# Kernel optimization log

Measured on AMD Instinct MI355X. Metric: run time of the kernel, lower is better.

Reference implementation:

```python
import jax, jax.numpy as jnp
import numpy as np
import math

HIDDEN = 4096
NUM_HEADS = 32
HEAD_DIM = HIDDEN // NUM_HEADS  # 128
SCALE = 1.0 / HEAD_DIM          # JAIS uses 1/d, not 1/sqrt(d)


def _alibi_slopes(n_heads: int) -> np.ndarray:
    cp2 = 2 ** math.floor(math.log2(n_heads))
    base = 2 ** (-2 ** (-(math.log2(cp2) - 3)))
    slopes = base ** np.arange(1, cp2 + 1, dtype=np.float32)
    if cp2 != n_heads:
        extra_base = 2 ** (-2 ** (-(math.log2(2 * cp2) - 3)))
        n_rem = min(cp2, n_heads - cp2)
        extra = extra_base ** np.arange(1, 1 + 2 * n_rem, 2, dtype=np.float32)
        slopes = np.concatenate([slopes, extra])
    return slopes.astype(np.float32)


def setup_inputs() -> dict:
    key = jax.random.key(0)
    k1, k2, k3, k4, k5 = jax.random.split(key, 5)
    B, S = 2, 2048
    return {
        "hidden_states": jax.random.normal(k1, (B, S, HIDDEN), dtype=jnp.float32),
        "w_attn": jax.random.normal(k2, (HIDDEN, 3 * HIDDEN), dtype=jnp.float32) * 0.02,
        "b_attn": jnp.zeros((3 * HIDDEN,), dtype=jnp.float32),
        "w_proj": jax.random.normal(k3, (HIDDEN, HIDDEN), dtype=jnp.float32) * 0.02,
        "b_proj": jnp.zeros((HIDDEN,), dtype=jnp.float32),
    }


def reference(hidden_states, w_attn, b_attn, w_proj, b_proj):
    B, S, _ = hidden_states.shape
    H, D = NUM_HEADS, HEAD_DIM

    # c_attn: fused QKV projection
    qkv = hidden_states @ w_attn + b_attn            # [B, S, 3*HIDDEN]
    q, k, v = jnp.split(qkv, 3, axis=-1)
    q = q.reshape(B, S, H, D)
    k = k.reshape(B, S, H, D)
    v = v.reshape(B, S, H, D)

    # attention scores with 1/d scaling
    scores = jnp.einsum("bqhd,bkhd->bhqk", q, k) * SCALE  # [B, H, S, S]

    # ALiBi bias: slope_h * (j - i), causal mask j <= i
    slopes = jnp.asarray(_alibi_slopes(H))                # [H]
    pos = jnp.arange(S)
    rel = pos[None, :] - pos[:, None]                     # j - i, [S, S]
    bias = slopes[:, None, None] * rel[None, :, :]        # [H, S, S]
    causal = rel <= 0
    scores = jnp.where(causal[None, None], scores + bias[None], -jnp.inf)

    attn = jax.nn.softmax(scores, axis=-1)
    out = jnp.einsum("bhqk,bkhd->bqhd", attn, v).reshape(B, S, HIDDEN)

    # c_proj
    return out @ w_proj + b_proj
```

## Files before the change

kernel.cpp:

```cpp
#include <hip/hip_runtime.h>
#include <hip/hip_bf16.h>
#include <cstdint>
#include <cstddef>

#define HIDDEN_ 4096
#define NHEAD 32
#define HDIM 128
#define SEQ 2048
#define BATCH 2
#define MROWS (BATCH * SEQ)
#define QKVN (3 * HIDDEN_)

typedef __bf16 bf16;
typedef __bf16 bf16x8 __attribute__((ext_vector_type(8)));
typedef float f32x4 __attribute__((ext_vector_type(4)));

#define AS1 __attribute__((address_space(1)))
#define AS3 __attribute__((address_space(3)))
#define PH_BAR do { asm volatile("" ::: "memory"); __builtin_amdgcn_s_barrier(); asm volatile("" ::: "memory"); } while (0)
#define MFMA_(d, a_, b_) (d) = __builtin_amdgcn_mfma_f32_16x16x32_bf16((a_), (b_), (d), 0, 0, 0)

__global__ __launch_bounds__(256) void cast_bf16_k(const float* __restrict__ in,
                                                   bf16* __restrict__ out, int n) {
  int i = (blockIdx.x * 256 + threadIdx.x) * 8;
  if (i >= n) return;
  f32x4 a = *(const f32x4*)(in + i);
  f32x4 b = *(const f32x4*)(in + i + 4);
  bf16x8 o;
  o[0] = (bf16)a[0]; o[1] = (bf16)a[1]; o[2] = (bf16)a[2]; o[3] = (bf16)a[3];
  o[4] = (bf16)b[0]; o[5] = (bf16)b[1]; o[6] = (bf16)b[2]; o[7] = (bf16)b[3];
  *(bf16x8*)(out + i) = o;
}

__global__ __launch_bounds__(256) void transpose_cast_k(const float* __restrict__ in,
                                                        bf16* __restrict__ out,
                                                        int R, int C) {
  __shared__ float tile[32][33];
  int c0 = blockIdx.x * 32, r0 = blockIdx.y * 32;
  int tx = threadIdx.x & 31, ty = threadIdx.x >> 5;
#pragma unroll
  for (int i = 0; i < 4; i++) {
    int r = ty + i * 8;
    tile[r][tx] = in[(size_t)(r0 + r) * C + (c0 + tx)];
  }
  __syncthreads();
#pragma unroll
  for (int i = 0; i < 4; i++) {
    int r = ty + i * 8;
    out[(size_t)(c0 + r) * R + (r0 + tx)] = (bf16)tile[tx][r];
  }
}

template <int EPI>
__global__ __launch_bounds__(512, 2) void gemm256_k(
    const bf16* __restrict__ A, const bf16* __restrict__ BT,
    const float* __restrict__ bias, float* __restrict__ outF,
    bf16* __restrict__ Qb, bf16* __restrict__ Kb, bf16* __restrict__ Vt,
    int M, int N, int K, int nbx) {
  __shared__ char lds[131072];
  char* const A0 = lds;
  char* const A1 = lds + 32768;
  char* const B0 = lds + 65536;
  char* const B1 = lds + 98304;

  const int tid = threadIdx.x;
  const int w = tid >> 6, l = tid & 63;
  const int lg = l >> 4, cl = l & 15;
  const int wm = (w >> 2) * 128;
  const int wn = (w & 3) * 64;

  const int cpx = (int)gridDim.x >> 3;
  const int bid = blockIdx.x;
  const int swz = (bid & 7) * cpx + (bid >> 3);
  const int bx = swz % nbx, by = swz / nbx;
  const int m0 = by * 256, n0 = bx * 256;

  const int NT = K >> 6;
  const int NI = K >> 7;

  const bf16* gA[2][2]; const bf16* gB[2][2];
#pragma unroll
  for (int half = 0; half < 2; ++half)
#pragma unroll
    for (int i = 0; i < 2; ++i) {
      const int ci = i * 512 + tid;
      const int r = ci >> 3;
      const int cb = ((ci & 7) << 4) ^ ((r & 7) << 4);
      gA[half][i] = A + (size_t)(m0 + half * 128 + r) * K + (cb >> 1);
      gB[half][i] = BT + (size_t)(n0 + half * 128 + r) * K + (cb >> 1);
    }

  int offA[8][2], offB[4][2];
#pragma unroll
  for (int mf = 0; mf < 8; ++mf) {
    const int r = wm + mf * 16 + cl;
#pragma unroll
    for (int ks = 0; ks < 2; ++ks)
      offA[mf][ks] = r * 128 + ((ks * 64 + lg * 16) ^ ((r & 7) << 4));
  }
#pragma unroll
  for (int nf = 0; nf < 4; ++nf) {
    const int r = wn + nf * 16 + cl;
#pragma unroll
    for (int ks = 0; ks < 2; ++ks)
      offB[nf][ks] = r * 128 + ((ks * 64 + lg * 16) ^ ((r & 7) << 4));
  }

  auto stageA = [&](char* buf, int half, int kt) {
#pragma unroll
    for (int i = 0; i < 2; ++i) {
      const int ci = i * 512 + tid;
      __builtin_amdgcn_global_load_lds((const AS1 void*)(gA[half][i] + kt * 64),
                                       (AS3 void*)(buf + half * 16384 + ci * 16), 16, 0, 0);
    }
  };
  auto stageB = [&](char* buf, int half, int kt) {
#pragma unroll
    for (int i = 0; i < 2; ++i) {
      const int ci = i * 512 + tid;
      __builtin_amdgcn_global_load_lds((const AS1 void*)(gB[half][i] + kt * 64),
                                       (AS3 void*)(buf + half * 16384 + ci * 16), 16, 0, 0);
    }
  };
  auto rdA = [&](const char* buf, int mf, int ks) -> bf16x8 {
    return *(const bf16x8*)(buf + offA[mf][ks]);
  };
  auto rdB = [&](const char* buf, int nf, int ks) -> bf16x8 {
    return *(const bf16x8*)(buf + offB[nf][ks]);
  };

  f32x4 acc[8][4] = {};
  bf16x8 alo[4][2], ahi[4][2], blo[2][2], bhi[2][2];

  stageA(A0, 0, 0); stageB(B0, 0, 0); stageA(A0, 1, 0); stageB(B0, 1, 0);
  stageB(B1, 0, 1); stageB(B1, 1, 1);
  asm volatile("s_waitcnt vmcnt(4)" ::: "memory");
  PH_BAR;

  for (int j = 0; j < NI; ++j) {
    const int tw = 2 * j + 1;
    const int tu = (2 * j + 2) & (NT - 1);
    const int tv = (2 * j + 3) & (NT - 1);

#pragma unroll
    for (int mf = 0; mf < 4; ++mf) { alo[mf][0] = rdA(A0, mf, 0); alo[mf][1] = rdA(A0, mf, 1); }
#pragma unroll
    for (int nf = 0; nf < 2; ++nf) { blo[nf][0] = rdB(B0, nf, 0); blo[nf][1] = rdB(B0, nf, 1); }
#pragma unroll
    for (int nf = 0; nf < 2; ++nf) { bhi[nf][0] = rdB(B0, 2 + nf, 0); bhi[nf][1] = rdB(B0, 2 + nf, 1); }
    stageA(A1, 0, tw);
    stageA(A1, 1, tw);
    __builtin_amdgcn_s_setprio(1);
#pragma unroll
    for (int mf = 0; mf < 4; ++mf)
#pragma unroll
      for (int nf = 0; nf < 2; ++nf)
#pragma unroll
        for (int ks = 0; ks < 2; ++ks) MFMA_(acc[mf][nf], alo[mf][ks], blo[nf][ks]);
#pragma unroll
    for (int mf = 0; mf < 4; ++mf)
#pragma unroll
      for (int nf = 0; nf < 2; ++nf)
#pragma unroll
        for (int ks = 0; ks < 2; ++ks) MFMA_(acc[mf][2 + nf], alo[mf][ks], bhi[nf][ks]);
    __builtin_amdgcn_s_setprio(0);
    PH_BAR;

#pragma unroll
    for (int mf = 0; mf < 4; ++mf) { ahi[mf][0] = rdA(A0, 4 + mf, 0); ahi[mf][1] = rdA(A0, 4 + mf, 1); }
    stageB(B0, 0, tu);
    stageB(B0, 1, tu);
    __builtin_amdgcn_s_setprio(1);
#pragma unroll
    for (int mf = 0; mf < 4; ++mf)
#pragma unroll
      for (int nf = 0; nf < 2; ++nf)
#pragma unroll
        for (int ks = 0; ks < 2; ++ks) MFMA_(acc[4 + mf][2 + nf], ahi[mf][ks], bhi[nf][ks]);
#pragma unroll
    for (int mf = 0; mf < 4; ++mf)
#pragma unroll
      for (int nf = 0; nf < 2; ++nf)
#pragma unroll
        for (int ks = 0; ks < 2; ++ks) MFMA_(acc[4 + mf][nf], ahi[mf][ks], blo[nf][ks]);
    __builtin_amdgcn_s_setprio(0);
    asm volatile("s_waitcnt vmcnt(4)" ::: "memory");
    PH_BAR;

#pragma unroll
    for (int mf = 0; mf < 4; ++mf) { alo[mf][0] = rdA(A1, mf, 0); alo[mf][1] = rdA(A1, mf, 1); }
#pragma unroll
    for (int nf = 0; nf < 2; ++nf) { blo[nf][0] = rdB(B1, nf, 0); blo[nf][1] = rdB(B1, nf, 1); }
#pragma unroll
    for (int nf = 0; nf < 2; ++nf) { bhi[nf][0] = rdB(B1, 2 + nf, 0); bhi[nf][1] = rdB(B1, 2 + nf, 1); }
    stageA(A0, 0, tu);
    stageA(A0, 1, tu);
    __builtin_amdgcn_s_setprio(1);
#pragma unroll
    for (int mf = 0; mf < 4; ++mf)
#pragma unroll
      for (int nf = 0; nf < 2; ++nf)
#pragma unroll
        for (int ks = 0; ks < 2; ++ks) MFMA_(acc[mf][nf], alo[mf][ks], blo[nf][ks]);
#pragma unroll
    for (int mf = 0; mf < 4; ++mf)
#pragma unroll
      for (int nf = 0; nf < 2; ++nf)
#pragma unroll
        for (int ks = 0; ks < 2; ++ks) MFMA_(acc[mf][2 + nf], alo[mf][ks], bhi[nf][ks]);
    __builtin_amdgcn_s_setprio(0);
    PH_BAR;

#pragma unroll
    for (int mf = 0; mf < 4; ++mf) { ahi[mf][0] = rdA(A1, 4 + mf, 0); ahi[mf][1] = rdA(A1, 4 + mf, 1); }
    stageB(B1, 0, tv);
    stageB(B1, 1, tv);
    __builtin_amdgcn_s_setprio(1);
#pragma unroll
    for (int mf = 0; mf < 4; ++mf)
#pragma unroll
      for (int nf = 0; nf < 2; ++nf)
#pragma unroll
        for (int ks = 0; ks < 2; ++ks) MFMA_(acc[4 + mf][2 + nf], ahi[mf][ks], bhi[nf][ks]);
#pragma unroll
    for (int mf = 0; mf < 4; ++mf)
#pragma unroll
      for (int nf = 0; nf < 2; ++nf)
#pragma unroll
        for (int ks = 0; ks < 2; ++ks) MFMA_(acc[4 + mf][nf], ahi[mf][ks], blo[nf][ks]);
    __builtin_amdgcn_s_setprio(0);
    asm volatile("s_waitcnt vmcnt(4)" ::: "memory");
    PH_BAR;
  }

#pragma unroll
  for (int mf = 0; mf < 8; ++mf) {
#pragma unroll
    for (int nf = 0; nf < 4; ++nf) {
      const int col = n0 + wn + nf * 16 + cl;
      const float bv = bias[col];
#pragma unroll
      for (int r = 0; r < 4; ++r) {
        const int row = m0 + wm + mf * 16 + lg * 4 + r;
        const float v = acc[mf][nf][r] + bv;
        if (EPI == 0) {
          const int which = col >> 12, rem = col & 4095;
          const int h = rem >> 7, d = rem & 127;
          const int b = row >> 11, s = row & 2047;
          const size_t bh = (size_t)b * NHEAD + h;
          if (which == 0)      Qb[(bh * SEQ + s) * HDIM + d] = (bf16)v;
          else if (which == 1) Kb[(bh * SEQ + s) * HDIM + d] = (bf16)v;
          else                 Vt[(bh * HDIM + d) * SEQ + s] = (bf16)v;
        } else {
          outF[(size_t)row * N + col] = v;
        }
      }
    }
  }
}

__global__ __launch_bounds__(512, 2) void attn_k(const bf16* __restrict__ Qb,
                                                 const bf16* __restrict__ Kb,
                                                 const bf16* __restrict__ Vt,
                                                 bf16* __restrict__ ctx) {
  __shared__ bf16 Ks[2][64 * 128];
  __shared__ bf16 Vs[2][128 * 64];
  __shared__ bf16 Pl[8][16 * 64];
  const int tid = threadIdx.x, w = tid >> 6, l = tid & 63;
  const int bid = blockIdx.x;
  const int qt = 15 - (bid >> 6);
  const int bh = bid & 63;
  const int h = bh & (NHEAD - 1), b = bh >> 5;
  const int qbase = qt * 128 + w * 16;
  const int nt = 2 * qt + 2;
  const float slope = exp2f(-0.25f * (float)(h + 1));
  const float scale = 1.0f / 128.0f;
  const int lg = l >> 4, cl = l & 15;

  const bf16* Qp = Qb + (size_t)bh * SEQ * HDIM;
  const bf16* Kp = Kb + (size_t)bh * SEQ * HDIM;
  const bf16* Vp = Vt + (size_t)bh * HDIM * SEQ;
  char* plb = (char*)&Pl[w][0];

  bf16x8 qf[4];
#pragma unroll
  for (int kb = 0; kb < 4; kb++)
    qf[kb] = *(const bf16x8*)&Qp[(size_t)(qbase + cl) * HDIM + kb * 32 + lg * 8];

  float mi[4], li[4];
#pragma unroll
  for (int r = 0; r < 4; r++) { mi[r] = -3.0e38f; li[r] = 0.0f; }
  f32x4 oacc[8] = {};

  auto stage = [&](int buf, int t) {
    const int kv0 = t * 64;
#pragma unroll
    for (int i = 0; i < 2; i++) {
      const int ci = i * 512 + tid;
      {
        const int r = ci >> 4;
        const int cbl = ((ci & 15) << 4) ^ ((r & 7) << 4);
        const bf16* src = Kp + (size_t)(kv0 + r) * HDIM + (cbl >> 1);
        __builtin_amdgcn_global_load_lds(
            (const AS1 void*)src,
            (AS3 void*)((char*)&Ks[buf][0] + ci * 16), 16, 0, 0);
      }
      {
        const int r = ci >> 3;
        const int cbl = ((ci & 7) << 4) ^ ((r & 7) << 4);
        const bf16* src = Vp + (size_t)r * SEQ + kv0 + (cbl >> 1);
        __builtin_amdgcn_global_load_lds(
            (const AS1 void*)src,
            (AS3 void*)((char*)&Vs[buf][0] + ci * 16), 16, 0, 0);
      }
    }
  };

  stage(0, 0);
  __syncthreads();

  for (int t = 0; t < nt; ++t) {
    const int cur = t & 1;
    if (t + 1 < nt) stage(cur ^ 1, t + 1);
    const int kv0 = t * 64;

    if (kv0 <= qbase + 15) {
      char* ksb = (char*)&Ks[cur][0];
      char* vsb = (char*)&Vs[cur][0];
      f32x4 sacc[4];
#pragma unroll
      for (int nb = 0; nb < 4; nb++) {
        f32x4 a = {};
#pragma unroll
        for (int kb = 0; kb < 4; kb++) {
          const int row = nb * 16 + cl;
          const int cb = (kb * 64 + lg * 16) ^ ((row & 7) << 4);
          bf16x8 kf = *(const bf16x8*)(ksb + row * 256 + cb);
          a = __builtin_amdgcn_mfma_f32_16x16x32_bf16(qf[kb], kf, a, 0, 0, 0);
        }
        sacc[nb] = a;
      }
      float pm[4], sv[4][4];
#pragma unroll
      for (int r = 0; r < 4; r++) pm[r] = -3.0e38f;
#pragma unroll
      for (int nb = 0; nb < 4; nb++) {
        const int kv = kv0 + nb * 16 + cl;
#pragma unroll
        for (int r = 0; r < 4; r++) {
          const int q = qbase + lg * 4 + r;
          float v = sacc[nb][r] * scale + slope * (float)(kv - q);
          v = (kv <= q) ? v : -3.0e38f;
          sv[nb][r] = v;
          pm[r] = fmaxf(pm[r], v);
        }
      }
#pragma unroll
      for (int r = 0; r < 4; r++) {
        pm[r] = fmaxf(pm[r], __shfl_xor(pm[r], 1));
        pm[r] = fmaxf(pm[r], __shfl_xor(pm[r], 2));
        pm[r] = fmaxf(pm[r], __shfl_xor(pm[r], 4));
        pm[r] = fmaxf(pm[r], __shfl_xor(pm[r], 8));
      }
      float alpha[4], rs[4];
#pragma unroll
      for (int r = 0; r < 4; r++) {
        const float nm = fmaxf(mi[r], pm[r]);
        alpha[r] = __expf(mi[r] - nm);
        mi[r] = nm;
        rs[r] = 0.0f;
      }
#pragma unroll
      for (int nb = 0; nb < 4; nb++) {
#pragma unroll
        for (int r = 0; r < 4; r++) {
          const float p = __expf(sv[nb][r] - mi[r]);
          rs[r] += p;
          const int row = lg * 4 + r;
          *(bf16*)(plb + row * 128 + ((((nb * 16 + cl) << 1)) ^ ((row & 7) << 4))) = (bf16)p;
        }
      }
#pragma unroll
      for (int r = 0; r < 4; r++) {
        rs[r] += __shfl_xor(rs[r], 1);
        rs[r] += __shfl_xor(rs[r], 2);
        rs[r] += __shfl_xor(rs[r], 4);
        rs[r] += __shfl_xor(rs[r], 8);
        li[r] = li[r] * alpha[r] + rs[r];
      }
#pragma unroll
      for (int db = 0; db < 8; db++)
#pragma unroll
        for (int r = 0; r < 4; r++) oacc[db][r] *= alpha[r];
      bf16x8 pa[2];
#pragma unroll
      for (int ks = 0; ks < 2; ks++) {
        const int cb = (ks * 64 + lg * 16) ^ ((cl & 7) << 4);
        pa[ks] = *(const bf16x8*)(plb + cl * 128 + cb);
      }
#pragma unroll
      for (int db = 0; db < 8; db++) {
        f32x4 o = oacc[db];
#pragma unroll
        for (int ks = 0; ks < 2; ks++) {
          const int row = db * 16 + cl;
          const int cb = (ks * 64 + lg * 16) ^ ((row & 7) << 4);
          bf16x8 vf = *(const bf16x8*)(vsb + row * 128 + cb);
          o = __builtin_amdgcn_mfma_f32_16x16x32_bf16(pa[ks], vf, o, 0, 0, 0);
        }
        oacc[db] = o;
      }
    }
    __syncthreads();
  }

  float inv[4];
#pragma unroll
  for (int r = 0; r < 4; r++) inv[r] = 1.0f / li[r];
#pragma unroll
  for (int db = 0; db < 8; db++) {
#pragma unroll
    for (int r = 0; r < 4; r++) {
      const int q = qbase + lg * 4 + r;
      ctx[((size_t)(b * SEQ + q)) * HIDDEN_ + h * HDIM + db * 16 + cl] = (bf16)(oacc[db][r] * inv[r]);
    }
  }
}

extern "C" void kernel_launch(void* const* d_in, const int* in_sizes, int n_in,
                              void* d_out, int out_size, void* d_ws, size_t ws_size,
                              hipStream_t stream) {
  const float* hs     = (const float*)d_in[0];
  const float* w_attn = (const float*)d_in[1];
  const float* b_attn = (const float*)d_in[2];
  const float* w_proj = (const float*)d_in[3];
  const float* b_proj = (const float*)d_in[4];
  float* out = (float*)d_out;

  char* ws = (char*)d_ws;
  bf16* Xb  = (bf16*)(ws + 0);
  bf16* WaT = (bf16*)(ws + 33554432);
  bf16* WpT = (bf16*)(ws + 134217728);
  bf16* Qb  = (bf16*)(ws + 167772160);
  bf16* Kb  = (bf16*)(ws + 201326592);
  bf16* Vt  = (bf16*)(ws + 234881024);
  bf16* ctx = (bf16*)(ws + 268435456);

  cast_bf16_k<<<(MROWS * HIDDEN_) / (256 * 8), 256, 0, stream>>>(hs, Xb, MROWS * HIDDEN_);
  transpose_cast_k<<<dim3(QKVN / 32, HIDDEN_ / 32), 256, 0, stream>>>(w_attn, WaT, HIDDEN_, QKVN);
  transpose_cast_k<<<dim3(HIDDEN_ / 32, HIDDEN_ / 32), 256, 0, stream>>>(w_proj, WpT, HIDDEN_, HIDDEN_);

  gemm256_k<0><<<dim3((QKVN / 256) * (MROWS / 256)), 512, 0, stream>>>(
      Xb, WaT, b_attn, nullptr, Qb, Kb, Vt, MROWS, QKVN, HIDDEN_, QKVN / 256);

  attn_k<<<16 * 64, 512, 0, stream>>>(Qb, Kb, Vt, ctx);

  gemm256_k<1><<<dim3((HIDDEN_ / 256) * (MROWS / 256)), 512, 0, stream>>>(
      ctx, WpT, b_proj, out, nullptr, nullptr, nullptr, MROWS, HIDDEN_, HIDDEN_, HIDDEN_ / 256);
}
```

Before: 767.3 us.

## Restructure GEMM mainloop to triple-buffered A with one barrier per K-tile

```diff
diff --git a/kernel.cpp b/kernel.cpp
--- a/kernel.cpp
+++ b/kernel.cpp
@@ -57,11 +57,7 @@
     const float* __restrict__ bias, float* __restrict__ outF,
     bf16* __restrict__ Qb, bf16* __restrict__ Kb, bf16* __restrict__ Vt,
     int M, int N, int K, int nbx) {
-  __shared__ char lds[131072];
-  char* const A0 = lds;
-  char* const A1 = lds + 32768;
-  char* const B0 = lds + 65536;
-  char* const B1 = lds + 98304;
+  __shared__ char lds[163840];
 
   const int tid = threadIdx.x;
   const int w = tid >> 6, l = tid & 63;
@@ -76,7 +72,6 @@
   const int m0 = by * 256, n0 = bx * 256;
 
   const int NT = K >> 6;
-  const int NI = K >> 7;
 
   const bf16* gA[2][2]; const bf16* gB[2][2];
 #pragma unroll
@@ -106,131 +101,74 @@
       offB[nf][ks] = r * 128 + ((ks * 64 + lg * 16) ^ ((r & 7) << 4));
   }
 
-  auto stageA = [&](char* buf, int half, int kt) {
-#pragma unroll
-    for (int i = 0; i < 2; ++i) {
-      const int ci = i * 512 + tid;
-      __builtin_amdgcn_global_load_lds((const AS1 void*)(gA[half][i] + kt * 64),
-                                       (AS3 void*)(buf + half * 16384 + ci * 16), 16, 0, 0);
-    }
+  auto stageA = [&](char* buf, int kt) {
+#pragma unroll
+    for (int half = 0; half < 2; ++half)
+#pragma unroll
+      for (int i = 0; i < 2; ++i) {
+        const int ci = i * 512 + tid;
+        __builtin_amdgcn_global_load_lds((const AS1 void*)(gA[half][i] + kt * 64),
+                                         (AS3 void*)(buf + half * 16384 + ci * 16), 16, 0, 0);
+      }
   };
-  auto stageB = [&](char* buf, int half, int kt) {
-#pragma unroll
-    for (int i = 0; i < 2; ++i) {
-      const int ci = i * 512 + tid;
-      __builtin_amdgcn_global_load_lds((const AS1 void*)(gB[half][i] + kt * 64),
-                                       (AS3 void*)(buf + half * 16384 + ci * 16), 16, 0, 0);
-    }
+  auto stageB = [&](char* buf, int kt) {
+#pragma unroll
+    for (int half = 0; half < 2; ++half)
+#pragma unroll
+      for (int i = 0; i < 2; ++i) {
+        const int ci = i * 512 + tid;
+        __builtin_amdgcn_global_load_lds((const AS1 void*)(gB[half][i] + kt * 64),
+                                         (AS3 void*)(buf + half * 16384 + ci * 16), 16, 0, 0);
+      }
   };
-  auto rdA = [&](const char* buf, int mf, int ks) -> bf16x8 {
-    return *(const bf16x8*)(buf + offA[mf][ks]);
-  };
-  auto rdB = [&](const char* buf, int nf, int ks) -> bf16x8 {
-    return *(const bf16x8*)(buf + offB[nf][ks]);
-  };
 
   f32x4 acc[8][4] = {};
-  bf16x8 alo[4][2], ahi[4][2], blo[2][2], bhi[2][2];
-
-  stageA(A0, 0, 0); stageB(B0, 0, 0); stageA(A0, 1, 0); stageB(B0, 1, 0);
-  stageB(B1, 0, 1); stageB(B1, 1, 1);
+
+  char* Ar0 = lds;
+  char* Ar1 = lds + 32768;
+  char* Ar2 = lds + 65536;
+  char* Br0 = lds + 98304;
+  char* Br1 = lds + 131072;
+
+  stageA(Ar0, 0);
+  stageB(Br0, 0);
+  stageA(Ar1, 1);
   asm volatile("s_waitcnt vmcnt(4)" ::: "memory");
   PH_BAR;
 
-  for (int j = 0; j < NI; ++j) {
-    const int tw = 2 * j + 1;
-    const int tu = (2 * j + 2) & (NT - 1);
-    const int tv = (2 * j + 3) & (NT - 1);
-
-#pragma unroll
-    for (int mf = 0; mf < 4; ++mf) { alo[mf][0] = rdA(A0, mf, 0); alo[mf][1] = rdA(A0, mf, 1); }
-#pragma unroll
-    for (int nf = 0; nf < 2; ++nf) { blo[nf][0] = rdB(B0, nf, 0); blo[nf][1] = rdB(B0, nf, 1); }
-#pragma unroll
-    for (int nf = 0; nf < 2; ++nf) { bhi[nf][0] = rdB(B0, 2 + nf, 0); bhi[nf][1] = rdB(B0, 2 + nf, 1); }
-    stageA(A1, 0, tw);
-    stageA(A1, 1, tw);
+  for (int t = 0; t < NT; ++t) {
+    if (t + 1 < NT) stageB(Br1, t + 1);
+    if (t + 2 < NT) stageA(Ar2, t + 2);
+
+    bf16x8 af[8][2], bf_[4][2];
+#pragma unroll
+    for (int mf = 0; mf < 8; ++mf) {
+      af[mf][0] = *(const bf16x8*)(Ar0 + offA[mf][0]);
+      af[mf][1] = *(const bf16x8*)(Ar0 + offA[mf][1]);
+    }
+#pragma unroll
+    for (int nf = 0; nf < 4; ++nf) {
+      bf_[nf][0] = *(const bf16x8*)(Br0 + offB[nf][0]);
+      bf_[nf][1] = *(const bf16x8*)(Br0 + offB[nf][1]);
+    }
     __builtin_amdgcn_s_setprio(1);
 #pragma unroll
-    for (int mf = 0; mf < 4; ++mf)
-#pragma unroll
-      for (int nf = 0; nf < 2; ++nf)
-#pragma unroll
-        for (int ks = 0; ks < 2; ++ks) MFMA_(acc[mf][nf], alo[mf][ks], blo[nf][ks]);
-#pragma unroll
-    for (int mf = 0; mf < 4; ++mf)
-#pragma unroll
-      for (int nf = 0; nf < 2; ++nf)
-#pragma unroll
-        for (int ks = 0; ks < 2; ++ks) MFMA_(acc[mf][2 + nf], alo[mf][ks], bhi[nf][ks]);
+    for (int mf = 0; mf < 8; ++mf)
+#pragma unroll
+      for (int nf = 0; nf < 4; ++nf)
+#pragma unroll
+        for (int ks = 0; ks < 2; ++ks) MFMA_(acc[mf][nf], af[mf][ks], bf_[nf][ks]);
     __builtin_amdgcn_s_setprio(0);
+
+    if (t + 2 < NT) {
+      asm volatile("s_waitcnt vmcnt(4)" ::: "memory");
+    } else {
+      asm volatile("s_waitcnt vmcnt(0)" ::: "memory");
+    }
     PH_BAR;
 
-#pragma unroll
-    for (int mf = 0; mf < 4; ++mf) { ahi[mf][0] = rdA(A0, 4 + mf, 0); ahi[mf][1] = rdA(A0, 4 + mf, 1); }
-    stageB(B0, 0, tu);
-    stageB(B0, 1, tu);
-    __builtin_amdgcn_s_setprio(1);
-#pragma unroll
-    for (int mf = 0; mf < 4; ++mf)
-#pragma unroll
-      for (int nf = 0; nf < 2; ++nf)
-#pragma unroll
-        for (int ks = 0; ks < 2; ++ks) MFMA_(acc[4 + mf][2 + nf], ahi[mf][ks], bhi[nf][ks]);
-#pragma unroll
-    for (int mf = 0; mf < 4; ++mf)
-#pragma unroll
-      for (int nf = 0; nf < 2; ++nf)
-#pragma unroll
-        for (int ks = 0; ks < 2; ++ks) MFMA_(acc[4 + mf][nf], ahi[mf][ks], blo[nf][ks]);
-    __builtin_amdgcn_s_setprio(0);
-    asm volatile("s_waitcnt vmcnt(4)" ::: "memory");
-    PH_BAR;
-
-#pragma unroll
-    for (int mf = 0; mf < 4; ++mf) { alo[mf][0] = rdA(A1, mf, 0); alo[mf][1] = rdA(A1, mf, 1); }
-#pragma unroll
-    for (int nf = 0; nf < 2; ++nf) { blo[nf][0] = rdB(B1, nf, 0); blo[nf][1] = rdB(B1, nf, 1); }
-#pragma unroll
-    for (int nf = 0; nf < 2; ++nf) { bhi[nf][0] = rdB(B1, 2 + nf, 0); bhi[nf][1] = rdB(B1, 2 + nf, 1); }
-    stageA(A0, 0, tu);
-    stageA(A0, 1, tu);
-    __builtin_amdgcn_s_setprio(1);
-#pragma unroll
-    for (int mf = 0; mf < 4; ++mf)
-#pragma unroll
-      for (int nf = 0; nf < 2; ++nf)
-#pragma unroll
-        for (int ks = 0; ks < 2; ++ks) MFMA_(acc[mf][nf], alo[mf][ks], blo[nf][ks]);
-#pragma unroll
-    for (int mf = 0; mf < 4; ++mf)
-#pragma unroll
-      for (int nf = 0; nf < 2; ++nf)
-#pragma unroll
-        for (int ks = 0; ks < 2; ++ks) MFMA_(acc[mf][2 + nf], alo[mf][ks], bhi[nf][ks]);
-    __builtin_amdgcn_s_setprio(0);
-    PH_BAR;
-
-#pragma unroll
-    for (int mf = 0; mf < 4; ++mf) { ahi[mf][0] = rdA(A1, 4 + mf, 0); ahi[mf][1] = rdA(A1, 4 + mf, 1); }
-    stageB(B1, 0, tv);
-    stageB(B1, 1, tv);
-    __builtin_amdgcn_s_setprio(1);
-#pragma unroll
-    for (int mf = 0; mf < 4; ++mf)
-#pragma unroll
-      for (int nf = 0; nf < 2; ++nf)
-#pragma unroll
-        for (int ks = 0; ks < 2; ++ks) MFMA_(acc[4 + mf][2 + nf], ahi[mf][ks], bhi[nf][ks]);
-#pragma unroll
-    for (int mf = 0; mf < 4; ++mf)
-#pragma unroll
-      for (int nf = 0; nf < 2; ++nf)
-#pragma unroll
-        for (int ks = 0; ks < 2; ++ks) MFMA_(acc[4 + mf][nf], ahi[mf][ks], blo[nf][ks]);
-    __builtin_amdgcn_s_setprio(0);
-    asm volatile("s_waitcnt vmcnt(4)" ::: "memory");
-    PH_BAR;
+    char* tmp = Ar0; Ar0 = Ar1; Ar1 = Ar2; Ar2 = tmp;
+    char* tb = Br0; Br0 = Br1; Br1 = tb;
   }
 
 #pragma unroll
```

Measured after the change: 785.0 us. 2.3% more time.

## Process 32 query rows per wave in attention to reuse K/V fragments

Applied to the files above, without the earlier changes.

```diff
diff --git a/kernel.cpp b/kernel.cpp
--- a/kernel.cpp
+++ b/kernel.cpp
@@ -259,19 +259,19 @@
   }
 }
 
-__global__ __launch_bounds__(512, 2) void attn_k(const bf16* __restrict__ Qb,
+__global__ __launch_bounds__(256, 2) void attn_k(const bf16* __restrict__ Qb,
                                                  const bf16* __restrict__ Kb,
                                                  const bf16* __restrict__ Vt,
                                                  bf16* __restrict__ ctx) {
   __shared__ bf16 Ks[2][64 * 128];
   __shared__ bf16 Vs[2][128 * 64];
-  __shared__ bf16 Pl[8][16 * 64];
+  __shared__ bf16 Pl[4][32 * 64];
   const int tid = threadIdx.x, w = tid >> 6, l = tid & 63;
   const int bid = blockIdx.x;
   const int qt = 15 - (bid >> 6);
   const int bh = bid & 63;
   const int h = bh & (NHEAD - 1), b = bh >> 5;
-  const int qbase = qt * 128 + w * 16;
+  const int qbase = qt * 128 + w * 32;
   const int nt = 2 * qt + 2;
   const float slope = exp2f(-0.25f * (float)(h + 1));
   const float scale = 1.0f / 128.0f;
@@ -282,21 +282,25 @@
   const bf16* Vp = Vt + (size_t)bh * HDIM * SEQ;
   char* plb = (char*)&Pl[w][0];
 
-  bf16x8 qf[4];
-#pragma unroll
-  for (int kb = 0; kb < 4; kb++)
-    qf[kb] = *(const bf16x8*)&Qp[(size_t)(qbase + cl) * HDIM + kb * 32 + lg * 8];
-
-  float mi[4], li[4];
-#pragma unroll
-  for (int r = 0; r < 4; r++) { mi[r] = -3.0e38f; li[r] = 0.0f; }
-  f32x4 oacc[8] = {};
+  bf16x8 qf[2][4];
+#pragma unroll
+  for (int mfr = 0; mfr < 2; ++mfr)
+#pragma unroll
+    for (int kb = 0; kb < 4; ++kb)
+      qf[mfr][kb] = *(const bf16x8*)&Qp[(size_t)(qbase + mfr * 16 + cl) * HDIM + kb * 32 + lg * 8];
+
+  float mi[2][4], li[2][4];
+#pragma unroll
+  for (int mfr = 0; mfr < 2; ++mfr)
+#pragma unroll
+    for (int r = 0; r < 4; ++r) { mi[mfr][r] = -3.0e38f; li[mfr][r] = 0.0f; }
+  f32x4 oacc[2][8] = {};
 
   auto stage = [&](int buf, int t) {
     const int kv0 = t * 64;
 #pragma unroll
-    for (int i = 0; i < 2; i++) {
-      const int ci = i * 512 + tid;
+    for (int i = 0; i < 4; i++) {
+      const int ci = i * 256 + tid;
       {
         const int r = ci >> 4;
         const int cbl = ((ci & 15) << 4) ^ ((r & 7) << 4);
@@ -324,105 +328,117 @@
     if (t + 1 < nt) stage(cur ^ 1, t + 1);
     const int kv0 = t * 64;
 
-    if (kv0 <= qbase + 15) {
+    if (kv0 <= qbase + 31) {
       char* ksb = (char*)&Ks[cur][0];
       char* vsb = (char*)&Vs[cur][0];
-      f32x4 sacc[4];
+      f32x4 sacc[2][4] = {};
+      __builtin_amdgcn_s_setprio(1);
 #pragma unroll
       for (int nb = 0; nb < 4; nb++) {
-        f32x4 a = {};
 #pragma unroll
         for (int kb = 0; kb < 4; kb++) {
           const int row = nb * 16 + cl;
           const int cb = (kb * 64 + lg * 16) ^ ((row & 7) << 4);
           bf16x8 kf = *(const bf16x8*)(ksb + row * 256 + cb);
-          a = __builtin_amdgcn_mfma_f32_16x16x32_bf16(qf[kb], kf, a, 0, 0, 0);
-        }
-        sacc[nb] = a;
-      }
-      float pm[4], sv[4][4];
-#pragma unroll
-      for (int r = 0; r < 4; r++) pm[r] = -3.0e38f;
-#pragma unroll
-      for (int nb = 0; nb < 4; nb++) {
-        const int kv = kv0 + nb * 16 + cl;
+#pragma unroll
+          for (int mfr = 0; mfr < 2; ++mfr)
+            sacc[mfr][nb] = __builtin_amdgcn_mfma_f32_16x16x32_bf16(qf[mfr][kb], kf, sacc[mfr][nb], 0, 0, 0);
+        }
+      }
+      __builtin_amdgcn_s_setprio(0);
+#pragma unroll
+      for (int mfr = 0; mfr < 2; ++mfr) {
+        float pm[4];
+#pragma unroll
+        for (int r = 0; r < 4; r++) pm[r] = -3.0e38f;
+#pragma unroll
+        for (int nb = 0; nb < 4; nb++) {
+          const int kv = kv0 + nb * 16 + cl;
+#pragma unroll
+          for (int r = 0; r < 4; r++) {
+            const int q = qbase + mfr * 16 + lg * 4 + r;
+            float v = sacc[mfr][nb][r] * scale + slope * (float)(kv - q);
+            v = (kv <= q) ? v : -3.0e38f;
+            sacc[mfr][nb][r] = v;
+            pm[r] = fmaxf(pm[r], v);
+          }
+        }
 #pragma unroll
         for (int r = 0; r < 4; r++) {
-          const int q = qbase + lg * 4 + r;
-          float v = sacc[nb][r] * scale + slope * (float)(kv - q);
-          v = (kv <= q) ? v : -3.0e38f;
-          sv[nb][r] = v;
-          pm[r] = fmaxf(pm[r], v);
-        }
-      }
-#pragma unroll
-      for (int r = 0; r < 4; r++) {
-        pm[r] = fmaxf(pm[r], __shfl_xor(pm[r], 1));
-        pm[r] = fmaxf(pm[r], __shfl_xor(pm[r], 2));
-        pm[r] = fmaxf(pm[r], __shfl_xor(pm[r], 4));
-        pm[r] = fmaxf(pm[r], __shfl_xor(pm[r], 8));
-      }
-      float alpha[4], rs[4];
-#pragma unroll
-      for (int r = 0; r < 4; r++) {
-        const float nm = fmaxf(mi[r], pm[r]);
-        alpha[r] = __expf(mi[r] - nm);
-        mi[r] = nm;
-        rs[r] = 0.0f;
-      }
-#pragma unroll
-      for (int nb = 0; nb < 4; nb++) {
+          pm[r] = fmaxf(pm[r], __shfl_xor(pm[r], 1));
+          pm[r] = fmaxf(pm[r], __shfl_xor(pm[r], 2));
+          pm[r] = fmaxf(pm[r], __shfl_xor(pm[r], 4));
+          pm[r] = fmaxf(pm[r], __shfl_xor(pm[r], 8));
+        }
+        float alpha[4], rs[4];
 #pragma unroll
         for (int r = 0; r < 4; r++) {
-          const float p = __expf(sv[nb][r] - mi[r]);
-          rs[r] += p;
-          const int row = lg * 4 + r;
-          *(bf16*)(plb + row * 128 + ((((nb * 16 + cl) << 1)) ^ ((row & 7) << 4))) = (bf16)p;
-        }
-      }
-#pragma unroll
-      for (int r = 0; r < 4; r++) {
-        rs[r] += __shfl_xor(rs[r], 1);
-        rs[r] += __shfl_xor(rs[r], 2);
-        rs[r] += __shfl_xor(rs[r], 4);
-        rs[r] += __shfl_xor(rs[r], 8);
-        li[r] = li[r] * alpha[r] + rs[r];
-      }
-#pragma unroll
-      for (int db = 0; db < 8; db++)
-#pragma unroll
-        for (int r = 0; r < 4; r++) oacc[db][r] *= alpha[r];
-      bf16x8 pa[2];
-#pragma unroll
-      for (int ks = 0; ks < 2; ks++) {
-        const int cb = (ks * 64 + lg * 16) ^ ((cl & 7) << 4);
-        pa[ks] = *(const bf16x8*)(plb + cl * 128 + cb);
-      }
+          const float nm = fmaxf(mi[mfr][r], pm[r]);
+          alpha[r] = __expf(mi[mfr][r] - nm);
+          mi[mfr][r] = nm;
+          rs[r] = 0.0f;
+        }
+#pragma unroll
+        for (int nb = 0; nb < 4; nb++) {
+#pragma unroll
+          for (int r = 0; r < 4; r++) {
+            const float p = __expf(sacc[mfr][nb][r] - mi[mfr][r]);
+            rs[r] += p;
+            const int row = mfr * 16 + lg * 4 + r;
+            *(bf16*)(plb + row * 128 + ((((nb * 16 + cl) << 1)) ^ ((row & 7) << 4))) = (bf16)p;
+          }
+        }
+#pragma unroll
+        for (int r = 0; r < 4; r++) {
+          rs[r] += __shfl_xor(rs[r], 1);
+          rs[r] += __shfl_xor(rs[r], 2);
+          rs[r] += __shfl_xor(rs[r], 4);
+          rs[r] += __shfl_xor(rs[r], 8);
+          li[mfr][r] = li[mfr][r] * alpha[r] + rs[r];
+        }
+#pragma unroll
+        for (int db = 0; db < 8; db++)
+#pragma unroll
+          for (int r = 0; r < 4; r++) oacc[mfr][db][r] *= alpha[r];
+      }
+      bf16x8 pa[2][2];
+#pragma unroll
+      for (int mfr = 0; mfr < 2; ++mfr)
+#pragma unroll
+        for (int ks = 0; ks < 2; ks++) {
+          const int cb = (ks * 64 + lg * 16) ^ ((cl & 7) << 4);
+          pa[mfr][ks] = *(const bf16x8*)(plb + (mfr * 16 + cl) * 128 + cb);
+        }
+      __builtin_amdgcn_s_setprio(1);
 #pragma unroll
       for (int db = 0; db < 8; db++) {
-        f32x4 o = oacc[db];
 #pragma unroll
         for (int ks = 0; ks < 2; ks++) {
           const int row = db * 16 + cl;
           const int cb = (ks * 64 + lg * 16) ^ ((row & 7) << 4);
           bf16x8 vf = *(const bf16x8*)(vsb + row * 128 + cb);
-          o = __builtin_amdgcn_mfma_f32_16x16x32_bf16(pa[ks], vf, o, 0, 0, 0);
-        }
-        oacc[db] = o;
-      }
+#pragma unroll
+          for (int mfr = 0; mfr < 2; ++mfr)
+            oacc[mfr][db] = __builtin_amdgcn_mfma_f32_16x16x32_bf16(pa[mfr][ks], vf, oacc[mfr][db], 0, 0, 0);
+        }
+      }
+      __builtin_amdgcn_s_setprio(0);
     }
     __syncthreads();
   }
 
-  float inv[4];
-#pragma unroll
-  for (int r = 0; r < 4; r++) inv[r] = 1.0f / li[r];
-#pragma unroll
-  for (int db = 0; db < 8; db++) {
-#pragma unroll
-    for (int r = 0; r < 4; r++) {
-      const int q = qbase + lg * 4 + r;
-      ctx[((size_t)(b * SEQ + q)) * HIDDEN_ + h * HDIM + db * 16 + cl] = (bf16)(oacc[db][r] * inv[r]);
+#pragma unroll
+  for (int mfr = 0; mfr < 2; ++mfr) {
+    float inv[4];
+#pragma unroll
+    for (int r = 0; r < 4; r++) inv[r] = 1.0f / li[mfr][r];
+#pragma unroll
+    for (int db = 0; db < 8; db++) {
+#pragma unroll
+      for (int r = 0; r < 4; r++) {
+        const int q = qbase + mfr * 16 + lg * 4 + r;
+        ctx[((size_t)(b * SEQ + q)) * HIDDEN_ + h * HDIM + db * 16 + cl] = (bf16)(oacc[mfr][db][r] * inv[r]);
+      }
     }
   }
 }
@@ -453,7 +469,7 @@
   gemm256_k<0><<<dim3((QKVN / 256) * (MROWS / 256)), 512, 0, stream>>>(
       Xb, WaT, b_attn, nullptr, Qb, Kb, Vt, MROWS, QKVN, HIDDEN_, QKVN / 256);
 
-  attn_k<<<16 * 64, 512, 0, stream>>>(Qb, Kb, Vt, ctx);
+  attn_k<<<16 * 64, 256, 0, stream>>>(Qb, Kb, Vt, ctx);
 
   gemm256_k<1><<<dim3((HIDDEN_ / 256) * (MROWS / 256)), 512, 0, stream>>>(
       ctx, WpT, b_proj, out, nullptr, nullptr, nullptr, MROWS, HIDDEN_, HIDDEN_, HIDDEN_ / 256);
```

Measured after the change: 758.7 us. Within noise of the previous version (-1.1%).
